# Performance work log

Measured on AMD Instinct MI355X. Metric: run time of the kernel, lower is better.

The kernel has to match this reference:

```python
import jax, jax.numpy as jnp
import numpy as np

KERNEL = 5
DILATIONS = (3, 1)
N_HEADS = 8
LN_EPS = 1e-5


def unfold1d(x, kernel, dilation, pad):
    # x: (N, H, S) -> (N, H, S, kernel) dilated sliding windows (same length)
    xp = jnp.pad(x, ((0, 0), (0, 0), (pad, pad)))
    S = x.shape[-1]
    idx = jnp.arange(S)[:, None] + jnp.arange(kernel)[None, :] * dilation  # (S, K)
    return xp[:, :, idx]  # (N, H, S, K)


def dilated_mha(q, k, v, Ws, bs, Wo, bo):
    # q,k,v: (B, S, D); Ws: (2, split, split); Wo: (D, D)
    B, S, D = q.shape
    ndil = len(DILATIONS)
    hpd = N_HEADS // ndil            # heads per dilation
    dk = D // N_HEADS
    split = D // ndil
    scale = dk ** (-0.5)
    outs, probs = [], []
    for i, dil in enumerate(DILATIONS):
        pad = dil * (KERNEL - 1) // 2
        sl = slice(i * split, (i + 1) * split)
        qi = q[..., sl] @ Ws[i].T + bs[i]
        ki = k[..., sl] @ Ws[i].T + bs[i]
        vi = v[..., sl] @ Ws[i].T + bs[i]
        # (B,S,hpd,dk) -> (B,dk,hpd,S), matching torch transpose(1,2).permute(0,3,1,2)
        to4 = lambda x: jnp.transpose(x.reshape(B, S, hpd, dk), (0, 3, 2, 1))
        qi4, ki4, vi4 = to4(qi), to4(ki), to4(vi)
        # unfold then reinterpret (B*dk,hpd,...) as (B*hpd,dk,...) exactly as torch .reshape does
        kp = unfold1d(ki4.reshape(B * dk, hpd, S), KERNEL, dil, pad).reshape(B * hpd, dk, S, KERNEL)
        vp = unfold1d(vi4.reshape(B * dk, hpd, S), KERNEL, dil, pad).reshape(B * hpd, dk, S, KERNEL)
        qr = qi4.reshape(B * hpd, dk, S)
        scores = jnp.einsum('nds,ndsk->nsk', qr, kp) * scale   # (B*hpd, S, K)
        p = jax.nn.softmax(scores, axis=-1)
        out = jnp.einsum('nsk,ndsk->nds', p, vp)               # (B*hpd, dk, S)
        out = jnp.transpose(out.reshape(B, hpd, dk, S), (0, 3, 1, 2)).reshape(B, S, split)
        outs.append(out)
        probs.append(p.reshape(B, hpd, S, KERNEL))
    o = jnp.concatenate(outs, axis=-1) @ Wo.T + bo
    return o, jnp.concatenate(probs, axis=1)


def layer_norm(x, g, b):
    mu = jnp.mean(x, axis=-1, keepdims=True)
    var = jnp.mean((x - mu) ** 2, axis=-1, keepdims=True)
    return (x - mu) * jax.lax.rsqrt(var + LN_EPS) * g + b


def setup_inputs() -> dict:
    key = jax.random.key(0)
    ks = jax.random.split(key, 6)
    B, S, D = 32, 2048, 256
    split = D // 2
    q_emb = jax.random.normal(ks[0], (B, S, D), dtype=jnp.float32)
    s_emb = jax.random.normal(ks[1], (B, S, D), dtype=jnp.float32)
    lens = jax.random.randint(ks[2], (B,), 5, S, dtype=jnp.int32)
    W_lin = jax.random.normal(ks[3], (3, 2, split, split), dtype=jnp.float32) * (split ** -0.5)
    b_lin = jnp.zeros((3, 2, split), dtype=jnp.float32)
    W_out = jax.random.normal(ks[4], (3, D, D), dtype=jnp.float32) * (D ** -0.5)
    b_out = jnp.zeros((3, D), dtype=jnp.float32)
    ln_g = jnp.ones((3, D), dtype=jnp.float32)
    ln_b = jnp.zeros((3, D), dtype=jnp.float32)
    return {"q_emb": q_emb, "s_emb": s_emb, "lens": lens, "W_lin": W_lin,
            "b_lin": b_lin, "W_out": W_out, "b_out": b_out, "ln_g": ln_g, "ln_b": ln_b}


def reference(q_emb, s_emb, lens, W_lin, b_lin, W_out, b_out, ln_g, ln_b):
    # CASTransformer.forward, shortcut=True path, eval mode (dropout=id, mask unused)
    a1, _ = dilated_mha(q_emb, q_emb, q_emb, W_lin[0], b_lin[0], W_out[0], b_out[0])
    hq = layer_norm(q_emb + a1, ln_g[0], ln_b[0])
    a2, q_scores = dilated_mha(s_emb, s_emb, s_emb, W_lin[1], b_lin[1], W_out[1], b_out[1])
    hs = layer_norm(s_emb + a2, ln_g[1], ln_b[1])
    a3, _ = dilated_mha(hq, hq, hs, W_lin[2], b_lin[2], W_out[2], b_out[2])
    z = layer_norm(hq + a3, ln_g[2], ln_b[2])
    return z, q_scores
```

## Files before the change

### kernel.cpp

```cpp
#include <hip/hip_runtime.h>
#include <hip/hip_bf16.h>

typedef __bf16 bf16x8 __attribute__((ext_vector_type(8)));
typedef float  f32x4  __attribute__((ext_vector_type(4)));
typedef unsigned int u32;
typedef u32 u32x4 __attribute__((ext_vector_type(4)));
typedef unsigned short ushort_t;

__device__ inline float bf2f(ushort_t h) {
    union { u32 u; float f; } v; v.u = ((u32)h) << 16; return v.f;
}
__device__ inline ushort_t f2bf(float f) {
    union { float f; u32 u; } v; v.f = f;
    u32 u = v.u;
    return (ushort_t)((u + 0x7fffu + ((u >> 16) & 1u)) >> 16);
}
__device__ inline bf16x8 load_bf8(const ushort_t* p) {
    u32x4 u = *reinterpret_cast<const u32x4*>(p);
    return __builtin_bit_cast(bf16x8, u);
}
__device__ inline bf16x8 load8_in(const void* base, size_t idx, int f32flag) {
    if (!f32flag) return load_bf8((const ushort_t*)base + idx);
    const float* pf = (const float*)base + idx;
    f32x4 a = *reinterpret_cast<const f32x4*>(pf);
    f32x4 b = *reinterpret_cast<const f32x4*>(pf + 4);
    bf16x8 r;
#pragma unroll
    for (int j = 0; j < 4; ++j) { r[j] = (__bf16)a[j]; r[4 + j] = (__bf16)b[j]; }
    return r;
}
__device__ inline float ld_in(const void* base, size_t idx, int f32flag) {
    return f32flag ? ((const float*)base)[idx] : bf2f(((const ushort_t*)base)[idx]);
}

__device__ inline int pofs(int row, int ch) { return row * 256 + (ch ^ ((row & 15) << 3)); }
__device__ inline int tofs(int tr, int ch) { return tr * 256 + (ch ^ (((tr + 8) & 15) << 3)); }

__device__ inline int f_of(const int* flags, int i) { return i < 0 ? 0 : flags[i]; }
__device__ inline int out_f32(const int* flags) {
    return flags[0] | flags[1] | flags[3] | flags[4] | flags[5] | flags[6] | flags[7] | flags[8];
}

__global__ __launch_bounds__(256) void detect_all(
    const u32* a0, const u32* a1, const u32* a2, const u32* a3,
    const u32* a4, const u32* a5, const u32* a6, const u32* a7,
    int* __restrict__ flags)
{
    const u32* arrs[8] = {a0, a1, a2, a3, a4, a5, a6, a7};
    const int  ns[8]   = {16384, 16384, 16384, 384, 16384, 384, 384, 384};
    const int  fi[8]   = {0, 1, 3, 4, 5, 6, 7, 8};
    const int  b = blockIdx.x;
    const u32* d = arrs[b];
    const int  n = ns[b];

    const int t = threadIdx.x;
    int cn = 0, co = 0;
    for (int i = t; i < n; i += 256) {
        const u32 w = d[i];
        const u32 e  = (w >> 7) & 0xFF;
        const u32 fe = (w >> 23) & 0xFF;
        cn += (e >= 100 && e <= 135) ? 1 : 0;
        co += (((w & 0xFFFFu) == 0u) && fe >= 100 && fe <= 140) ? 1 : 0;
    }
    __shared__ int sn[256], so[256];
    sn[t] = cn; so[t] = co; __syncthreads();
    for (int o = 128; o; o >>= 1) {
        if (t < o) { sn[t] += sn[t + o]; so[t] += so[t + o]; }
        __syncthreads();
    }
    if (t == 0) {
        const int CN = sn[0], CO = so[0];
        const int is_f32 = (2 * CN < n) && ((2 * CO > n) || (20 * CN > n));
        flags[fi[b]] = is_f32 ? 1 : 0;
    }
}

__global__ __launch_bounds__(256, 4) void proj2_kernel(
    const void* X0, int xi0, size_t lw0, size_t lb0, ushort_t* __restrict__ Y0,
    const void* X1, int xi1, size_t lw1, size_t lb1, ushort_t* __restrict__ Y1,
    const void* __restrict__ W, const void* __restrict__ Bv, const int* __restrict__ flags)
{
    __shared__ __align__(16) ushort_t tile[64 * 256];
    const int half = blockIdx.x >> 10;
    const void* X = half ? X1 : X0;
    const int   xi = half ? xi1 : xi0;
    const size_t lw = half ? lw1 : lw0;
    const size_t lb = half ? lb1 : lb0;
    ushort_t* Y = half ? Y1 : Y0;

    const int xf  = f_of(flags, xi);
    const int wf  = flags[3], bfl = flags[4];
    const int tid = threadIdx.x;
    const int m0  = (blockIdx.x & 1023) * 64;

#pragma unroll
    for (int i = 0; i < 8; ++i) {
        const int c = tid + 256 * i;
        const int row = c >> 5, cc = c & 31;
        bf16x8 v = load8_in(X, (size_t)(m0 + row) * 256 + cc * 8, xf);
        *reinterpret_cast<u32x4*>(&tile[pofs(row, cc * 8)]) = __builtin_bit_cast(u32x4, v);
    }
    __syncthreads();

    const int wave = tid >> 6, lane = tid & 63;
    const int dil  = wave >> 1;
    const int n_off = (wave & 1) * 64;
    const int l15  = lane & 15, quad = lane >> 4;

    f32x4 acc[4][4] = {};
    for (int kc = 0; kc < 4; ++kc) {
        bf16x8 a[4], b[4];
#pragma unroll
        for (int mt = 0; mt < 4; ++mt)
            a[mt] = load_bf8(&tile[pofs(mt * 16 + l15, dil * 128 + kc * 32 + quad * 8)]);
#pragma unroll
        for (int nt = 0; nt < 4; ++nt)
            b[nt] = load8_in(W, lw + (size_t)dil * 16384 +
                             (size_t)(n_off + nt * 16 + l15) * 128 + kc * 32 + quad * 8, wf);
#pragma unroll
        for (int mt = 0; mt < 4; ++mt)
#pragma unroll
            for (int nt = 0; nt < 4; ++nt)
                acc[mt][nt] = __builtin_amdgcn_mfma_f32_16x16x32_bf16(a[mt], b[nt], acc[mt][nt], 0, 0, 0);
    }
    __syncthreads();

#pragma unroll
    for (int nt = 0; nt < 4; ++nt) {
        const int ncol = n_off + nt * 16 + l15;
        const float bias = ld_in(Bv, lb + dil * 128 + ncol, bfl);
#pragma unroll
        for (int mt = 0; mt < 4; ++mt)
#pragma unroll
            for (int r = 0; r < 4; ++r) {
                const int row = mt * 16 + quad * 4 + r;
                tile[pofs(row, dil * 128 + ncol)] = f2bf(acc[mt][nt][r] + bias);
            }
    }
    __syncthreads();

#pragma unroll
    for (int i = 0; i < 8; ++i) {
        const int c = tid + 256 * i;
        const int row = c >> 5, cc = c & 31;
        *reinterpret_cast<u32x4*>(Y + (size_t)(m0 + row) * 256 + cc * 8) =
            *reinterpret_cast<const u32x4*>(&tile[row * 256 + cc * 8]);
    }
}

__global__ __launch_bounds__(256, 4) void fused_attn_oln_kernel(
    const ushort_t* __restrict__ P, const ushort_t* __restrict__ V,
    const void* __restrict__ R, int ri,
    const void* __restrict__ W, size_t lw,
    const void* __restrict__ Bv, size_t lb,
    const void* __restrict__ G, const void* __restrict__ Bt, size_t lg,
    void* __restrict__ H, int h_out,
    void* __restrict__ probs_base,
    const int* __restrict__ flags)
{
    __shared__ ushort_t tile[80 * 256];
    float (*lsum)[64] = (float (*)[64])(&tile[0]);
    float (*lsq)[64]  = (float (*)[64])(&tile[1024]);

    const int wf = flags[5], bvf = flags[6], gf = flags[7], btf = flags[8];
    const int rf = f_of(flags, ri);
    const int og = out_f32(flags);
    const int of = h_out ? og : 0;

    const int tid  = threadIdx.x;
    const int wave = tid >> 6, lane = tid & 63;
    const int l15  = lane & 15, quad = lane >> 4;
    const int m0   = blockIdx.x * 64;
    const int bb   = m0 >> 11;
    const int s0   = m0 & 2047;
    const size_t rowbase = (size_t)bb * 2048;
    const float scale = 0.17677669529663687f;

#pragma unroll
    for (int i = 0; i < 10; ++i) {
        const int c = tid + 256 * i;
        const int tr = c >> 5, cc = c & 31;
        int s = s0 - 8 + tr; s = s < 0 ? 0 : (s > 2047 ? 2047 : s);
        *reinterpret_cast<u32x4*>(&tile[tr * 256 + cc * 8]) =
            *reinterpret_cast<const u32x4*>(P + (rowbase + s) * 256 + cc * 8);
    }
    __syncthreads();

    const int r = lane, g = wave;
    const int s = s0 + r;

    float p2[2][5];
#pragma unroll
    for (int it = 0; it < 2; ++it) {
        const int dil  = it;
        const int dila = dil ? 1 : 3;
        const int ch0  = dil * 128 + g * 8;

        float qv[4][8];
#pragma unroll
        for (int h = 0; h < 4; ++h) {
            bf16x8 t = load_bf8(&tile[tofs(8 + r, ch0 + h * 32)]);
#pragma unroll
            for (int j = 0; j < 8; ++j) qv[h][j] = (float)t[j];
        }
        float sc[5];
#pragma unroll
        for (int kk = 0; kk < 5; ++kk) {
            const int sp = s + (kk - 2) * dila;
            float a = 0.f;
            if (sp >= 0 && sp < 2048) {
                const int tr2 = 8 + r + (kk - 2) * dila;
#pragma unroll
                for (int h = 0; h < 4; ++h) {
                    bf16x8 t = load_bf8(&tile[tofs(tr2, ch0 + h * 32)]);
#pragma unroll
                    for (int j = 0; j < 8; ++j) a += qv[h][j] * (float)t[j];
                }
                a *= scale;
            }
            sc[kk] = a;
        }
        float mx = sc[0];
#pragma unroll
        for (int kk = 1; kk < 5; ++kk) mx = fmaxf(mx, sc[kk]);
        float sum = 0.f;
#pragma unroll
        for (int kk = 0; kk < 5; ++kk) { p2[it][kk] = __expf(sc[kk] - mx); sum += p2[it][kk]; }
        const float inv = 1.f / sum;
#pragma unroll
        for (int kk = 0; kk < 5; ++kk) p2[it][kk] *= inv;

        if (probs_base != nullptr) {
            const size_t pb = 16777216 + ((size_t)((bb * 8 + dil * 4 + g) * 2048 + s)) * 5;
            if (og) {
                float* pp = (float*)probs_base;
#pragma unroll
                for (int kk = 0; kk < 5; ++kk) pp[pb + kk] = p2[it][kk];
            } else {
                ushort_t* pp = (ushort_t*)probs_base;
#pragma unroll
                for (int kk = 0; kk < 5; ++kk) pp[pb + kk] = f2bf(p2[it][kk]);
            }
        }
    }

    if (V != P) {
        __syncthreads();
#pragma unroll
        for (int i = 0; i < 10; ++i) {
            const int c = tid + 256 * i;
            const int tr = c >> 5, cc = c & 31;
            int s2 = s0 - 8 + tr; s2 = s2 < 0 ? 0 : (s2 > 2047 ? 2047 : s2);
            *reinterpret_cast<u32x4*>(&tile[tr * 256 + cc * 8]) =
                *reinterpret_cast<const u32x4*>(V + (rowbase + s2) * 256 + cc * 8);
        }
        __syncthreads();
    }

    u32x4 wpk[2][4];
#pragma unroll
    for (int it = 0; it < 2; ++it) {
        const int dil  = it;
        const int dila = dil ? 1 : 3;
        const int ch0  = dil * 128 + g * 8;
        float o[4][8] = {};
#pragma unroll
        for (int kk = 0; kk < 5; ++kk) {
            const int sp = s + (kk - 2) * dila;
            if (sp < 0 || sp >= 2048) continue;
            const int tr2 = 8 + r + (kk - 2) * dila;
#pragma unroll
            for (int h = 0; h < 4; ++h) {
                bf16x8 t = load_bf8(&tile[tofs(tr2, ch0 + h * 32)]);
#pragma unroll
                for (int j = 0; j < 8; ++j) o[h][j] += p2[it][kk] * (float)t[j];
            }
        }
#pragma unroll
        for (int c = 0; c < 4; ++c) {
            u32x4 w;
#pragma unroll
            for (int t4 = 0; t4 < 4; ++t4) {
                const int d2a = c * 8 + t4 * 2, d2b = d2a + 1;
                const u32 lo = f2bf(o[d2a & 3][d2a >> 2]);
                const u32 hi = f2bf(o[d2b & 3][d2b >> 2]);
                w[t4] = lo | (hi << 16);
            }
            wpk[it][c] = w;
        }
    }
    __syncthreads();

#pragma unroll
    for (int it = 0; it < 2; ++it)
#pragma unroll
        for (int c = 0; c < 4; ++c)
            *reinterpret_cast<u32x4*>(&tile[tofs(8 + r, it * 128 + g * 32 + c * 8)]) = wpk[it][c];
    __syncthreads();

    const int n_off = wave * 64;

    f32x4 acc[4][4] = {};
    for (int kc = 0; kc < 8; ++kc) {
        bf16x8 a[4], b[4];
#pragma unroll
        for (int mt = 0; mt < 4; ++mt)
            a[mt] = load_bf8(&tile[tofs(8 + mt * 16 + l15, kc * 32 + quad * 8)]);
#pragma unroll
        for (int nt = 0; nt < 4; ++nt)
            b[nt] = load8_in(W, lw + (size_t)(n_off + nt * 16 + l15) * 256 + kc * 32 + quad * 8, wf);
#pragma unroll
        for (int mt = 0; mt < 4; ++mt)
#pragma unroll
            for (int nt = 0; nt < 4; ++nt)
                acc[mt][nt] = __builtin_amdgcn_mfma_f32_16x16x32_bf16(a[mt], b[nt], acc[mt][nt], 0, 0, 0);
    }

    float bias[4];
#pragma unroll
    for (int nt = 0; nt < 4; ++nt) bias[nt] = ld_in(Bv, lb + n_off + nt * 16 + l15, bvf);

    float psum[4][4] = {}, psq[4][4] = {};
#pragma unroll
    for (int mt = 0; mt < 4; ++mt) {
#pragma unroll
        for (int rr = 0; rr < 4; ++rr) {
            const size_t rrow = (size_t)(m0 + mt * 16 + quad * 4 + rr) * 256 + l15;
#pragma unroll
            for (int nt = 0; nt < 4; ++nt) {
                float v = acc[mt][nt][rr] + bias[nt] + ld_in(R, rrow + n_off + nt * 16, rf);
                acc[mt][nt][rr] = v;
                psum[mt][rr] += v;
                psq[mt][rr]  += v * v;
            }
        }
    }
#pragma unroll
    for (int off = 1; off <= 8; off <<= 1) {
#pragma unroll
        for (int mt = 0; mt < 4; ++mt)
#pragma unroll
            for (int rr = 0; rr < 4; ++rr) {
                psum[mt][rr] += __shfl_xor(psum[mt][rr], off);
                psq[mt][rr]  += __shfl_xor(psq[mt][rr],  off);
            }
    }
    if (l15 == 0) {
#pragma unroll
        for (int mt = 0; mt < 4; ++mt)
#pragma unroll
            for (int rr = 0; rr < 4; ++rr) {
                const int row = mt * 16 + quad * 4 + rr;
                lsum[wave][row] = psum[mt][rr];
                lsq[wave][row]  = psq[mt][rr];
            }
    }
    __syncthreads();

    float gl[4], blv[4];
#pragma unroll
    for (int nt = 0; nt < 4; ++nt) {
        gl[nt]  = ld_in(G,  lg + n_off + nt * 16 + l15, gf);
        blv[nt] = ld_in(Bt, lg + n_off + nt * 16 + l15, btf);
    }
#pragma unroll
    for (int mt = 0; mt < 4; ++mt) {
#pragma unroll
        for (int rr = 0; rr < 4; ++rr) {
            const int row = mt * 16 + quad * 4 + rr;
            const float sm = lsum[0][row] + lsum[1][row] + lsum[2][row] + lsum[3][row];
            const float q2 = lsq[0][row]  + lsq[1][row]  + lsq[2][row]  + lsq[3][row];
            const float mu  = sm * (1.f / 256.f);
            const float var = q2 * (1.f / 256.f) - mu * mu;
            const float rs  = rsqrtf(var + 1e-5f);
            const size_t hrow = (size_t)(m0 + row) * 256 + l15;
#pragma unroll
            for (int nt = 0; nt < 4; ++nt) {
                const float hv = (acc[mt][nt][rr] - mu) * rs * gl[nt] + blv[nt];
                if (of) ((float*)H)[hrow + n_off + nt * 16] = hv;
                else    ((ushort_t*)H)[hrow + n_off + nt * 16] = f2bf(hv);
            }
        }
    }
}

extern "C" void kernel_launch(void* const* d_in, const int* in_sizes, int n_in,
                              void* d_out, int out_size, void* d_ws, size_t ws_size,
                              hipStream_t stream) {
    const void* q_emb = d_in[0];
    const void* s_emb = d_in[1];
    const void* W_lin = d_in[3];
    const void* b_lin = d_in[4];
    const void* W_out = d_in[5];
    const void* b_out = d_in[6];
    const void* ln_g  = d_in[7];
    const void* ln_b  = d_in[8];

    const size_t SLOT = 16777216;
    int*      flags = (int*)d_ws;
    ushort_t* S1 = (ushort_t*)((char*)d_ws + 256);
    ushort_t* S2 = S1 + SLOT;
    ushort_t* S3 = S1 + 2 * SLOT;

    const dim3 blk(256);
    detect_all<<<8, blk, 0, stream>>>((const u32*)q_emb, (const u32*)s_emb, (const u32*)W_lin,
        (const u32*)b_lin, (const u32*)W_out, (const u32*)b_out,
        (const u32*)ln_g, (const u32*)ln_b, flags);

    proj2_kernel<<<2048, blk, 0, stream>>>(q_emb, 0, 0, 0, S1,
                                           s_emb, 1, 32768, 256, S2,
                                           W_lin, b_lin, flags);
    fused_attn_oln_kernel<<<1024, blk, 0, stream>>>(S1, S1, q_emb, 0,
        W_out, 0, b_out, 0, ln_g, ln_b, 0, S3, 0, nullptr, flags);
    fused_attn_oln_kernel<<<1024, blk, 0, stream>>>(S2, S2, s_emb, 1,
        W_out, 65536, b_out, 256, ln_g, ln_b, 256, S1, 0, d_out, flags);
    proj2_kernel<<<2048, blk, 0, stream>>>(S3, -1, 65536, 512, S2,
                                           S1, -1, 65536, 512, S1,
                                           W_lin, b_lin, flags);
    fused_attn_oln_kernel<<<1024, blk, 0, stream>>>(S2, S1, S3, -1,
        W_out, 131072, b_out, 512, ln_g, ln_b, 512, d_out, 1, nullptr, flags);
}
```

Baseline: 558.5 us.

## Merge independent attention stages into one launch and stage LN output via LDS

The two independent first-layer attention+out-proj+LayerNorm stages now run as a single 2048-block launch, with each block choosing its parameter set from the high bit of blockIdx. This relies on a fourth workspace slot and falls back to separate launches when the workspace is too small. The LayerNorm epilogue now writes results into shared memory (swizzled for bf16, two 32-row halves for fp32) and then stores them with coalesced 16-byte vector writes, replacing scattered scalar stores. The trade-off is extra synchronisation and LDS traffic in the epilogue.

```diff
diff --git a/kernel.cpp b/kernel.cpp
--- a/kernel.cpp
+++ b/kernel.cpp
@@ -148,19 +148,30 @@
     }
 }
 
-__global__ __launch_bounds__(256, 4) void fused_attn_oln_kernel(
-    const ushort_t* __restrict__ P, const ushort_t* __restrict__ V,
-    const void* __restrict__ R, int ri,
-    const void* __restrict__ W, size_t lw,
-    const void* __restrict__ Bv, size_t lb,
-    const void* __restrict__ G, const void* __restrict__ Bt, size_t lg,
-    void* __restrict__ H, int h_out,
-    void* __restrict__ probs_base,
+__global__ __launch_bounds__(256, 4) void fused2_kernel(
+    const ushort_t* P0, const ushort_t* V0, const void* R0, int ri0,
+    size_t lw0, size_t lb0, size_t lg0, void* H0, int h0, void* pr0,
+    const ushort_t* P1, const ushort_t* V1, const void* R1, int ri1,
+    size_t lw1, size_t lb1, size_t lg1, void* H1, int h1, void* pr1,
+    const void* __restrict__ W, const void* __restrict__ Bv,
+    const void* __restrict__ G, const void* __restrict__ Bt,
     const int* __restrict__ flags)
 {
-    __shared__ ushort_t tile[80 * 256];
+    __shared__ __align__(16) ushort_t tile[80 * 256];
     float (*lsum)[64] = (float (*)[64])(&tile[0]);
     float (*lsq)[64]  = (float (*)[64])(&tile[1024]);
+
+    const int half = blockIdx.x >> 10;
+    const ushort_t* P = half ? P1 : P0;
+    const ushort_t* V = half ? V1 : V0;
+    const void* R  = half ? R1 : R0;
+    const int   ri = half ? ri1 : ri0;
+    const size_t lw = half ? lw1 : lw0;
+    const size_t lb = half ? lb1 : lb0;
+    const size_t lg = half ? lg1 : lg0;
+    void* H        = half ? H1 : H0;
+    const int h_out = half ? h1 : h0;
+    void* probs_base = half ? pr1 : pr0;
 
     const int wf = flags[5], bvf = flags[6], gf = flags[7], btf = flags[8];
     const int rf = f_of(flags, ri);
@@ -170,7 +181,7 @@
     const int tid  = threadIdx.x;
     const int wave = tid >> 6, lane = tid & 63;
     const int l15  = lane & 15, quad = lane >> 4;
-    const int m0   = blockIdx.x * 64;
+    const int m0   = (blockIdx.x & 1023) * 64;
     const int bb   = m0 >> 11;
     const int s0   = m0 & 2047;
     const size_t rowbase = (size_t)bb * 2048;
@@ -373,13 +384,56 @@
             const float mu  = sm * (1.f / 256.f);
             const float var = q2 * (1.f / 256.f) - mu * mu;
             const float rs  = rsqrtf(var + 1e-5f);
-            const size_t hrow = (size_t)(m0 + row) * 256 + l15;
-#pragma unroll
-            for (int nt = 0; nt < 4; ++nt) {
-                const float hv = (acc[mt][nt][rr] - mu) * rs * gl[nt] + blv[nt];
-                if (of) ((float*)H)[hrow + n_off + nt * 16] = hv;
-                else    ((ushort_t*)H)[hrow + n_off + nt * 16] = f2bf(hv);
-            }
+#pragma unroll
+            for (int nt = 0; nt < 4; ++nt)
+                acc[mt][nt][rr] = (acc[mt][nt][rr] - mu) * rs * gl[nt] + blv[nt];
+        }
+    }
+    __syncthreads();
+
+    if (of) {
+        float* tf = (float*)tile;
+#pragma unroll
+        for (int hh = 0; hh < 2; ++hh) {
+#pragma unroll
+            for (int mh = 0; mh < 2; ++mh) {
+                const int mt = 2 * hh + mh;
+#pragma unroll
+                for (int rr = 0; rr < 4; ++rr) {
+                    const int lrow = mh * 16 + quad * 4 + rr;
+#pragma unroll
+                    for (int nt = 0; nt < 4; ++nt)
+                        tf[lrow * 256 + n_off + nt * 16 + l15] = acc[mt][nt][rr];
+                }
+            }
+            __syncthreads();
+#pragma unroll
+            for (int i = 0; i < 8; ++i) {
+                const int c = tid + 256 * i;
+                const int row = c >> 6, cc = c & 63;
+                *reinterpret_cast<f32x4*>((float*)H + (size_t)(m0 + hh * 32 + row) * 256 + cc * 4) =
+                    *reinterpret_cast<const f32x4*>(&tf[row * 256 + cc * 4]);
+            }
+            __syncthreads();
+        }
+    } else {
+#pragma unroll
+        for (int mt = 0; mt < 4; ++mt)
+#pragma unroll
+            for (int rr = 0; rr < 4; ++rr) {
+                const int row = mt * 16 + quad * 4 + rr;
+#pragma unroll
+                for (int nt = 0; nt < 4; ++nt)
+                    tile[pofs(row, n_off + nt * 16 + l15)] = f2bf(acc[mt][nt][rr]);
+            }
+        __syncthreads();
+#pragma unroll
+        for (int i = 0; i < 8; ++i) {
+            const int c = tid + 256 * i;
+            const int row = c >> 5, cc = c & 31;
+            const int sc8 = (cc * 8) ^ ((row & 15) << 3);
+            *reinterpret_cast<u32x4*>((ushort_t*)H + (size_t)(m0 + row) * 256 + cc * 8) =
+                *reinterpret_cast<const u32x4*>(&tile[row * 256 + sc8]);
         }
     }
 }
@@ -401,6 +455,8 @@
     ushort_t* S1 = (ushort_t*)((char*)d_ws + 256);
     ushort_t* S2 = S1 + SLOT;
     ushort_t* S3 = S1 + 2 * SLOT;
+    ushort_t* S4 = S1 + 3 * SLOT;
+    const size_t need4 = 256 + 4 * SLOT * sizeof(ushort_t);
 
     const dim3 blk(256);
     detect_all<<<8, blk, 0, stream>>>((const u32*)q_emb, (const u32*)s_emb, (const u32*)W_lin,
@@ -410,13 +466,34 @@
     proj2_kernel<<<2048, blk, 0, stream>>>(q_emb, 0, 0, 0, S1,
                                            s_emb, 1, 32768, 256, S2,
                                            W_lin, b_lin, flags);
-    fused_attn_oln_kernel<<<1024, blk, 0, stream>>>(S1, S1, q_emb, 0,
-        W_out, 0, b_out, 0, ln_g, ln_b, 0, S3, 0, nullptr, flags);
-    fused_attn_oln_kernel<<<1024, blk, 0, stream>>>(S2, S2, s_emb, 1,
-        W_out, 65536, b_out, 256, ln_g, ln_b, 256, S1, 0, d_out, flags);
-    proj2_kernel<<<2048, blk, 0, stream>>>(S3, -1, 65536, 512, S2,
-                                           S1, -1, 65536, 512, S1,
-                                           W_lin, b_lin, flags);
-    fused_attn_oln_kernel<<<1024, blk, 0, stream>>>(S2, S1, S3, -1,
-        W_out, 131072, b_out, 512, ln_g, ln_b, 512, d_out, 1, nullptr, flags);
-}
+
+    if (ws_size >= need4) {
+        fused2_kernel<<<2048, blk, 0, stream>>>(
+            S1, S1, q_emb, 0, 0,     0,   0,   S3, 0, nullptr,
+            S2, S2, s_emb, 1, 65536, 256, 256, S4, 0, d_out,
+            W_out, b_out, ln_g, ln_b, flags);
+        proj2_kernel<<<2048, blk, 0, stream>>>(S3, -1, 65536, 512, S1,
+                                               S4, -1, 65536, 512, S2,
+                                               W_lin, b_lin, flags);
+        fused2_kernel<<<1024, blk, 0, stream>>>(
+            S1, S2, S3, -1, 131072, 512, 512, d_out, 1, nullptr,
+            S1, S2, S3, -1, 131072, 512, 512, d_out, 1, nullptr,
+            W_out, b_out, ln_g, ln_b, flags);
+    } else {
+        fused2_kernel<<<1024, blk, 0, stream>>>(
+            S1, S1, q_emb, 0, 0, 0, 0, S3, 0, nullptr,
+            S1, S1, q_emb, 0, 0, 0, 0, S3, 0, nullptr,
+            W_out, b_out, ln_g, ln_b, flags);
+        fused2_kernel<<<1024, blk, 0, stream>>>(
+            S2, S2, s_emb, 1, 65536, 256, 256, S1, 0, d_out,
+            S2, S2, s_emb, 1, 65536, 256, 256, S1, 0, d_out,
+            W_out, b_out, ln_g, ln_b, flags);
+        proj2_kernel<<<2048, blk, 0, stream>>>(S3, -1, 65536, 512, S2,
+                                               S1, -1, 65536, 512, S1,
+                                               W_lin, b_lin, flags);
+        fused2_kernel<<<1024, blk, 0, stream>>>(
+            S2, S1, S3, -1, 131072, 512, 512, d_out, 1, nullptr,
+            S2, S1, S3, -1, 131072, 512, 512, d_out, 1, nullptr,
+            W_out, b_out, ln_g, ln_b, flags);
+    }
+}
```

Measured after the change: 571.0 us. 1.02x slower.

## Give each wave its own row slice in projection kernel, removing block barriers

Applied to the files above, without the earlier changes.

The projection kernel now gives each of its four waves an independent 16-row slice of the 64-row block. Each wave stages its slice in a private LDS region and computes all 256 output columns for both dilations. This removes all __syncthreads from the kernel, so waves no longer stall on each other between load, MFMA and store. In exchange, every wave reads the full weight matrix from global memory or cache instead of a quarter of it, which raises weight traffic per block by four times. Register pressure also rises, with 16 accumulators per lane.

```diff
diff --git a/kernel.cpp b/kernel.cpp
--- a/kernel.cpp
+++ b/kernel.cpp
@@ -80,7 +80,7 @@
     const void* X1, int xi1, size_t lw1, size_t lb1, ushort_t* __restrict__ Y1,
     const void* __restrict__ W, const void* __restrict__ Bv, const int* __restrict__ flags)
 {
-    __shared__ __align__(16) ushort_t tile[64 * 256];
+    __shared__ __align__(16) ushort_t tile[4][16 * 256];
     const int half = blockIdx.x >> 10;
     const void* X = half ? X1 : X0;
     const int   xi = half ? xi1 : xi0;
@@ -91,60 +91,53 @@
     const int xf  = f_of(flags, xi);
     const int wf  = flags[3], bfl = flags[4];
     const int tid = threadIdx.x;
-    const int m0  = (blockIdx.x & 1023) * 64;
+    const int wave = tid >> 6, lane = tid & 63;
+    const int m0  = (blockIdx.x & 1023) * 64 + wave * 16;
+    ushort_t* wt = tile[wave];
 
 #pragma unroll
     for (int i = 0; i < 8; ++i) {
-        const int c = tid + 256 * i;
+        const int c = lane + 64 * i;
         const int row = c >> 5, cc = c & 31;
         bf16x8 v = load8_in(X, (size_t)(m0 + row) * 256 + cc * 8, xf);
-        *reinterpret_cast<u32x4*>(&tile[pofs(row, cc * 8)]) = __builtin_bit_cast(u32x4, v);
-    }
-    __syncthreads();
-
-    const int wave = tid >> 6, lane = tid & 63;
-    const int dil  = wave >> 1;
-    const int n_off = (wave & 1) * 64;
-    const int l15  = lane & 15, quad = lane >> 4;
-
-    f32x4 acc[4][4] = {};
-    for (int kc = 0; kc < 4; ++kc) {
-        bf16x8 a[4], b[4];
-#pragma unroll
-        for (int mt = 0; mt < 4; ++mt)
-            a[mt] = load_bf8(&tile[pofs(mt * 16 + l15, dil * 128 + kc * 32 + quad * 8)]);
-#pragma unroll
-        for (int nt = 0; nt < 4; ++nt)
-            b[nt] = load8_in(W, lw + (size_t)dil * 16384 +
-                             (size_t)(n_off + nt * 16 + l15) * 128 + kc * 32 + quad * 8, wf);
-#pragma unroll
-        for (int mt = 0; mt < 4; ++mt)
-#pragma unroll
-            for (int nt = 0; nt < 4; ++nt)
-                acc[mt][nt] = __builtin_amdgcn_mfma_f32_16x16x32_bf16(a[mt], b[nt], acc[mt][nt], 0, 0, 0);
-    }
-    __syncthreads();
-
-#pragma unroll
-    for (int nt = 0; nt < 4; ++nt) {
-        const int ncol = n_off + nt * 16 + l15;
-        const float bias = ld_in(Bv, lb + dil * 128 + ncol, bfl);
-#pragma unroll
-        for (int mt = 0; mt < 4; ++mt)
-#pragma unroll
-            for (int r = 0; r < 4; ++r) {
-                const int row = mt * 16 + quad * 4 + r;
-                tile[pofs(row, dil * 128 + ncol)] = f2bf(acc[mt][nt][r] + bias);
-            }
-    }
-    __syncthreads();
+        *reinterpret_cast<u32x4*>(&wt[pofs(row, cc * 8)]) = __builtin_bit_cast(u32x4, v);
+    }
+
+    const int l15 = lane & 15, quad = lane >> 4;
+
+    f32x4 acc[2][8] = {};
+#pragma unroll
+    for (int dil = 0; dil < 2; ++dil) {
+        for (int kc = 0; kc < 4; ++kc) {
+            bf16x8 a = load_bf8(&wt[pofs(l15, dil * 128 + kc * 32 + quad * 8)]);
+            bf16x8 b[8];
+#pragma unroll
+            for (int nt = 0; nt < 8; ++nt)
+                b[nt] = load8_in(W, lw + (size_t)dil * 16384 +
+                                 (size_t)(nt * 16 + l15) * 128 + kc * 32 + quad * 8, wf);
+#pragma unroll
+            for (int nt = 0; nt < 8; ++nt)
+                acc[dil][nt] = __builtin_amdgcn_mfma_f32_16x16x32_bf16(a, b[nt], acc[dil][nt], 0, 0, 0);
+        }
+    }
+
+#pragma unroll
+    for (int dil = 0; dil < 2; ++dil)
+#pragma unroll
+        for (int nt = 0; nt < 8; ++nt) {
+            const int ncol = nt * 16 + l15;
+            const float bias = ld_in(Bv, lb + dil * 128 + ncol, bfl);
+#pragma unroll
+            for (int r = 0; r < 4; ++r)
+                wt[pofs(quad * 4 + r, dil * 128 + ncol)] = f2bf(acc[dil][nt][r] + bias);
+        }
 
 #pragma unroll
     for (int i = 0; i < 8; ++i) {
-        const int c = tid + 256 * i;
+        const int c = lane + 64 * i;
         const int row = c >> 5, cc = c & 31;
         *reinterpret_cast<u32x4*>(Y + (size_t)(m0 + row) * 256 + cc * 8) =
-            *reinterpret_cast<const u32x4*>(&tile[row * 256 + cc * 8]);
+            *reinterpret_cast<const u32x4*>(&wt[row * 256 + cc * 8]);
     }
 }
 
```

New measurement: 729.8 us. 30.7% more time.
